# Optimization experiments

Measured on AMD Instinct MI355X. Metric: run time of the kernel, lower is better.

## Reference

```python
import jax, jax.numpy as jnp
import numpy as np

N_NODES = 100000


def gcn_conv(x, W, b, src, dst, n_nodes):
    # PyG GCNConv: h = x @ W; add self-loops; sym-normalized scatter-add; + bias
    loop = jnp.arange(n_nodes, dtype=src.dtype)
    src2 = jnp.concatenate([src, loop])
    dst2 = jnp.concatenate([dst, loop])
    deg = jax.ops.segment_sum(jnp.ones(src2.shape, x.dtype), dst2, num_segments=n_nodes)
    dinv = jax.lax.rsqrt(deg)  # deg >= 1 thanks to self-loops
    norm = dinv[src2] * dinv[dst2]                 # [E+N]
    h = x @ W                                      # [N, out]
    msg = h[src2] * norm[:, None]                  # gather + scale, [E+N, out]
    out = jax.ops.segment_sum(msg, dst2, num_segments=n_nodes)  # scatter-add
    return out + b


def setup_inputs() -> dict:
    key = jax.random.key(0)
    k1, k2, k3, k4, k5 = jax.random.split(key, 5)
    nfeat, nhid = 128, 64
    n_edges = 1600000
    x = jax.random.normal(k1, (N_NODES, nfeat), dtype=jnp.float32)
    edge_index = jax.random.randint(k2, (2, n_edges), 0, N_NODES, dtype=jnp.int64)
    W1 = jax.random.normal(k3, (nfeat, nhid), dtype=jnp.float32) / np.sqrt(nfeat)
    b1 = jnp.zeros((nhid,), jnp.float32)
    W2 = jax.random.normal(k4, (nhid, nhid), dtype=jnp.float32) / np.sqrt(nhid)
    b2 = jnp.zeros((nhid,), jnp.float32)
    return {"x": x, "edge_index": edge_index, "W1": W1, "b1": b1, "W2": W2, "b2": b2}


def reference(x, edge_index, W1, b1, W2, b2):
    # eval mode: dropout is identity
    src, dst = edge_index[0], edge_index[1]
    h = jax.nn.relu(gcn_conv(x, W1, b1, src, dst, N_NODES))
    residual = h
    out = jax.nn.relu(gcn_conv(h, W2, b2, src, dst, N_NODES))
    return out + residual
```

## Files before the change

kernel.cpp:

```cpp
#include <hip/hip_runtime.h>

#define N_NODES 100000
#define NDUMMY 100000
#define NH 64
#define NB 512
#define NPB 196
#define BCAP 4096
#define PBCAP 5760
#define EPB 8192


__device__ __forceinline__ unsigned short f2bf(float f) {
    union { float f; unsigned int i; } c;
    c.f = f;
    unsigned int b = c.i;
    b += 0x7FFFu + ((b >> 16) & 1u);
    return (unsigned short)(b >> 16);
}

__device__ __forceinline__ unsigned pack2bf(float lo, float hi) {
    return (unsigned)f2bf(lo) | ((unsigned)f2bf(hi) << 16);
}

__device__ __forceinline__ float bfLO(unsigned u) {
    union { unsigned i; float f; } c; c.i = u << 16; return c.f;
}
__device__ __forceinline__ float bfHI(unsigned u) {
    union { unsigned i; float f; } c; c.i = u & 0xFFFF0000u; return c.f;
}


__global__ __launch_bounds__(512) void k_init(int* __restrict__ bcur, unsigned* __restrict__ dummy_row) {
    int t = threadIdx.x;
    if (t < NB) bcur[t] = 0;
    if (t < 32) dummy_row[t] = 0;
}


__global__ __launch_bounds__(1024) void k_sort(const int* __restrict__ src, const int* __restrict__ dst,
                                               int* __restrict__ bcur, unsigned* __restrict__ ebuf, int e) {
    __shared__ unsigned sorted[EPB];
    __shared__ unsigned short cellof[EPB];
    __shared__ int lh[NB];
    __shared__ int lbase[NB];
    __shared__ int lcur[NB];
    __shared__ int gpos[NB];
    __shared__ int wsum[8];
    const int t = threadIdx.x;
    const int e0 = blockIdx.x * EPB;
    int cnt = e - e0; if (cnt > EPB) cnt = EPB;

    if (t < NB) lh[t] = 0;
    __syncthreads();

    for (int i = t * 4; i < cnt; i += 4096) {
        int4 d4 = *(const int4*)&dst[e0 + i];
        atomicAdd(&lh[d4.x / NPB], 1);
        atomicAdd(&lh[d4.y / NPB], 1);
        atomicAdd(&lh[d4.z / NPB], 1);
        atomicAdd(&lh[d4.w / NPB], 1);
    }
    __syncthreads();

    const int lane = t & 63, wave = t >> 6;
    int v = 0, inc = 0;
    if (t < NB) {
        v = lh[t];
        inc = v;
#pragma unroll
        for (int d = 1; d < 64; d <<= 1) {
            int u = __shfl_up(inc, d, 64);
            if (lane >= d) inc += u;
        }
        if (lane == 63) wsum[wave] = inc;
    }
    __syncthreads();
    if (t < NB) {
        int woff = 0;
#pragma unroll
        for (int w = 0; w < 8; ++w)
            if (w < wave) woff += wsum[w];
        const int excl = woff + inc - v;
        lbase[t] = excl;
        lcur[t] = excl;
        gpos[t] = atomicAdd(&bcur[t], v);
    }
    __syncthreads();

    for (int i = t * 4; i < cnt; i += 4096) {
        int4 d4 = *(const int4*)&dst[e0 + i];
        int4 s4 = *(const int4*)&src[e0 + i];
        int b0 = d4.x / NPB, b1 = d4.y / NPB, b2 = d4.z / NPB, b3 = d4.w / NPB;
        int p0 = atomicAdd(&lcur[b0], 1);
        int p1 = atomicAdd(&lcur[b1], 1);
        int p2 = atomicAdd(&lcur[b2], 1);
        int p3 = atomicAdd(&lcur[b3], 1);
        sorted[p0] = ((unsigned)(d4.x - b0 * NPB) << 17) | (unsigned)s4.x; cellof[p0] = (unsigned short)b0;
        sorted[p1] = ((unsigned)(d4.y - b1 * NPB) << 17) | (unsigned)s4.y; cellof[p1] = (unsigned short)b1;
        sorted[p2] = ((unsigned)(d4.z - b2 * NPB) << 17) | (unsigned)s4.z; cellof[p2] = (unsigned short)b2;
        sorted[p3] = ((unsigned)(d4.w - b3 * NPB) << 17) | (unsigned)s4.w; cellof[p3] = (unsigned short)b3;
    }
    __syncthreads();

    for (int i = t * 4; i < cnt; i += 4096) {
        uint4 sv = *(const uint4*)&sorted[i];
        ushort4 cv = *(const ushort4*)&cellof[i];
        int c0 = cv.x, c1 = cv.y, c2 = cv.z, c3 = cv.w;
        int g0 = gpos[c0] + (i + 0 - lbase[c0]);
        int g1 = gpos[c1] + (i + 1 - lbase[c1]);
        int g2 = gpos[c2] + (i + 2 - lbase[c2]);
        int g3 = gpos[c3] + (i + 3 - lbase[c3]);
        if (g0 < BCAP) ebuf[(long long)c0 * BCAP + g0] = sv.x;
        if (g1 < BCAP) ebuf[(long long)c1 * BCAP + g1] = sv.y;
        if (g2 < BCAP) ebuf[(long long)c2 * BCAP + g2] = sv.z;
        if (g3 < BCAP) ebuf[(long long)c3 * BCAP + g3] = sv.w;
    }
}

__global__ __launch_bounds__(256) void k_build(const unsigned* __restrict__ ebuf, const int* __restrict__ bcur,
                                               int* __restrict__ rowptr, int* __restrict__ degp,
                                               float* __restrict__ dinv, int* __restrict__ csrc, int n) {
    __shared__ unsigned ls[BCAP];
    __shared__ int lh[256];
    __shared__ int lpv[256];
    __shared__ int lstart[256];
    __shared__ int lc[256];
    __shared__ int wsum[4];
    const int b = blockIdx.x;
    const int t = threadIdx.x;
    const int node0 = b * NPB;
    int count = bcur[b];
    if (count > BCAP) count = BCAP;
    const int rbase = b * PBCAP;

    lh[t] = 0;
    for (int i = t; i < count; i += 256) ls[i] = ebuf[(long long)b * BCAP + i];
    __syncthreads();
    for (int i = t; i < count; i += 256) atomicAdd(&lh[ls[i] >> 17], 1);
    __syncthreads();

    const int v = lh[t];
    lpv[t] = (v + 7) & ~7;
    __syncthreads();
    const int g = t & ~3;
    const int pvg = max(max(lpv[g], lpv[g + 1]), max(lpv[g + 2], lpv[g + 3]));

    const int lane = t & 63, wave = t >> 6;
    int inc = pvg;
#pragma unroll
    for (int d = 1; d < 64; d <<= 1) {
        int u = __shfl_up(inc, d, 64);
        if (lane >= d) inc += u;
    }
    if (lane == 63) wsum[wave] = inc;
    __syncthreads();
    int woff = 0;
#pragma unroll
    for (int w = 0; w < 4; ++w)
        if (w < wave) woff += wsum[w];
    const int start = rbase + woff + inc - pvg;

    lstart[t] = start;
    lc[t] = start;
    const int node = node0 + t;
    if (t < NPB && node < n) {
        rowptr[node] = start;
        degp[node] = pvg;
        dinv[node] = rsqrtf((float)(v + 1));
    }
    __syncthreads();

    for (int i = t; i < count; i += 256) {
        unsigned u = ls[i];
        int pos = atomicAdd(&lc[u >> 17], 1);
        csrc[pos] = (int)(u & 0x1FFFFu);
    }
    __syncthreads();

    const int pend = lstart[t] + pvg;
    for (int p = lc[t]; p < pend; ++p) csrc[p] = NDUMMY;
}


template <int K>
__global__ __launch_bounds__(256) void k_gemm_scale(const float* __restrict__ X, const float* __restrict__ W,
                                                    const float* __restrict__ dinv,
                                                    unsigned short* __restrict__ out, int n) {
    __shared__ float xsT[64][68];
    __shared__ float ws[64][64];
    const int tid = threadIdx.x;
    const int n0 = blockIdx.x * 64;
    const int tc = tid & 15;
    const int tn = tid >> 4;

    float acc[4][4];
#pragma unroll
    for (int r = 0; r < 4; ++r)
#pragma unroll
        for (int c = 0; c < 4; ++c) acc[r][c] = 0.f;

    for (int kb = 0; kb < K; kb += 64) {
        for (int idx = tid * 4; idx < 4096; idx += 1024) {
            int r = idx >> 6, c = idx & 63;
            *(float4*)&ws[r][c] = *(const float4*)&W[(kb + r) * NH + c];
        }
        for (int idx = tid * 4; idx < 4096; idx += 1024) {
            int row = idx >> 6, c = idx & 63;
            float4 v = make_float4(0.f, 0.f, 0.f, 0.f);
            if (n0 + row < n) v = *(const float4*)&X[(long long)(n0 + row) * K + kb + c];
            xsT[c + 0][row] = v.x;
            xsT[c + 1][row] = v.y;
            xsT[c + 2][row] = v.z;
            xsT[c + 3][row] = v.w;
        }
        __syncthreads();

#pragma unroll 8
        for (int k = 0; k < 64; ++k) {
            float4 xa = *(const float4*)&xsT[k][tn * 4];
            float4 wa = *(const float4*)&ws[k][tc * 4];
            float xr[4] = {xa.x, xa.y, xa.z, xa.w};
            float wc[4] = {wa.x, wa.y, wa.z, wa.w};
#pragma unroll
            for (int r = 0; r < 4; ++r)
#pragma unroll
                for (int c = 0; c < 4; ++c) acc[r][c] += xr[r] * wc[c];
        }
        __syncthreads();
    }

#pragma unroll
    for (int r = 0; r < 4; ++r) {
        int node = n0 + 4 * tn + r;
        if (node < n) {
            float dv = dinv[node];
            ushort4 o;
            o.x = f2bf(acc[r][0] * dv);
            o.y = f2bf(acc[r][1] * dv);
            o.z = f2bf(acc[r][2] * dv);
            o.w = f2bf(acc[r][3] * dv);
            *(ushort4*)&out[(long long)node * NH + tc * 4] = o;
        }
    }
}


__global__ __launch_bounds__(256) void k_agg(const unsigned* __restrict__ hs32, const float* __restrict__ dinv,
                                             const int* __restrict__ rowptr, const int* __restrict__ degp,
                                             const int* __restrict__ csrc,
                                             const float* __restrict__ bias, const float* __restrict__ resid,
                                             float* __restrict__ out, int n) {
    const int gt = blockIdx.x * 256 + threadIdx.x;
    const int wave = gt >> 6;
    const int lane = threadIdx.x & 63;
    const int sub = lane >> 4;
    const int li = lane & 15;
    const int node = wave * 4 + sub;
    if (node >= n) return;

    const uint2* hsv = (const uint2*)hs32;
    uint2 su = hsv[node * 16 + li];
    float aLx = bfLO(su.x), aHx = bfHI(su.x), aLy = bfLO(su.y), aHy = bfHI(su.y);
    float bLx = 0.f, bHx = 0.f, bLy = 0.f, bHy = 0.f;

    const int rp = rowptr[node];
    const int dg = degp[node];
    for (int e = 0; e < dg; e += 8) {
        int4 c0 = *(const int4*)&csrc[rp + e];
        int4 c1 = *(const int4*)&csrc[rp + e + 4];
        uint2 u0 = hsv[c0.x * 16 + li];
        uint2 u1 = hsv[c0.y * 16 + li];
        uint2 u2 = hsv[c0.z * 16 + li];
        uint2 u3 = hsv[c0.w * 16 + li];
        uint2 u4 = hsv[c1.x * 16 + li];
        uint2 u5 = hsv[c1.y * 16 + li];
        uint2 u6 = hsv[c1.z * 16 + li];
        uint2 u7 = hsv[c1.w * 16 + li];
        aLx += bfLO(u0.x); aHx += bfHI(u0.x); aLy += bfLO(u0.y); aHy += bfHI(u0.y);
        bLx += bfLO(u1.x); bHx += bfHI(u1.x); bLy += bfLO(u1.y); bHy += bfHI(u1.y);
        aLx += bfLO(u2.x); aHx += bfHI(u2.x); aLy += bfLO(u2.y); aHy += bfHI(u2.y);
        bLx += bfLO(u3.x); bHx += bfHI(u3.x); bLy += bfLO(u3.y); bHy += bfHI(u3.y);
        aLx += bfLO(u4.x); aHx += bfHI(u4.x); aLy += bfLO(u4.y); aHy += bfHI(u4.y);
        bLx += bfLO(u5.x); bHx += bfHI(u5.x); bLy += bfLO(u5.y); bHy += bfHI(u5.y);
        aLx += bfLO(u6.x); aHx += bfHI(u6.x); aLy += bfLO(u6.y); aHy += bfHI(u6.y);
        bLx += bfLO(u7.x); bHx += bfHI(u7.x); bLy += bfLO(u7.y); bHy += bfHI(u7.y);
    }
    const float dv = dinv[node];
    const float4 bb = *(const float4*)&bias[4 * li];
    float v0 = fmaxf(dv * (aLx + bLx) + bb.x, 0.f);
    float v1 = fmaxf(dv * (aHx + bHx) + bb.y, 0.f);
    float v2 = fmaxf(dv * (aLy + bLy) + bb.z, 0.f);
    float v3 = fmaxf(dv * (aHy + bHy) + bb.w, 0.f);
    const long long ob = (long long)node * NH + 4 * li;
    if (resid) {
        float4 rr = *(const float4*)&resid[ob];
        v0 += rr.x; v1 += rr.y; v2 += rr.z; v3 += rr.w;
    }
    *(float4*)&out[ob] = make_float4(v0, v1, v2, v3);
}


extern "C" void kernel_launch(void* const* d_in, const int* in_sizes, int n_in,
                              void* d_out, int out_size, void* d_ws, size_t ws_size,
                              hipStream_t stream) {
    const float* x  = (const float*)d_in[0];
    const int*   ei = (const int*)d_in[1];
    const float* W1 = (const float*)d_in[2];
    const float* b1 = (const float*)d_in[3];
    const float* W2 = (const float*)d_in[4];
    const float* b2 = (const float*)d_in[5];
    float* out = (float*)d_out;

    const int N = N_NODES;
    const int E = in_sizes[1] / 2;
    const int* src = ei;
    const int* dst = ei + E;

    const int NP = 100352;
    int*   bcur   = (int*)d_ws;
    int*   rowptr = bcur + NB;
    int*   degp   = rowptr + NP;
    float* dinv   = (float*)(degp + NP);
    int*   csrc   = (int*)(dinv + NP);
    unsigned* ebuf = (unsigned*)(csrc + NB * PBCAP);
    unsigned* hs32 = ebuf;
    unsigned short* hsb = (unsigned short*)hs32;
    float* h1     = (float*)(hs32 + (long long)(NDUMMY + 1) * 32);

    const int nb_sort = (E + EPB - 1) / EPB;

    k_init<<<1, 512, 0, stream>>>(bcur, hs32 + (long long)NDUMMY * 32);
    k_sort<<<nb_sort, 1024, 0, stream>>>(src, dst, bcur, ebuf, E);
    k_build<<<NB, 256, 0, stream>>>(ebuf, bcur, rowptr, degp, dinv, csrc, N);

    k_gemm_scale<128><<<(N + 63) / 64, 256, 0, stream>>>(x, W1, dinv, hsb, N);
    k_agg<<<(N + 15) / 16, 256, 0, stream>>>(hs32, dinv, rowptr, degp, csrc, b1, nullptr, h1, N);

    k_gemm_scale<64><<<(N + 63) / 64, 256, 0, stream>>>(h1, W2, dinv, hsb, N);
    k_agg<<<(N + 15) / 16, 256, 0, stream>>>(hs32, dinv, rowptr, degp, csrc, b2, h1, out, N);
}
```

Measured before the change: 153.6 us.

## Replace FP32 SIMT GEMM with bf16 MFMA matrix-core GEMM

```diff
diff --git a/kernel.cpp b/kernel.cpp
--- a/kernel.cpp
+++ b/kernel.cpp
@@ -182,64 +182,80 @@
 }
 
 
+typedef __attribute__((ext_vector_type(8))) short bf16x8;
+typedef __attribute__((ext_vector_type(4))) float f32x4;
+
 template <int K>
-__global__ __launch_bounds__(256) void k_gemm_scale(const float* __restrict__ X, const float* __restrict__ W,
-                                                    const float* __restrict__ dinv,
-                                                    unsigned short* __restrict__ out, int n) {
-    __shared__ float xsT[64][68];
-    __shared__ float ws[64][64];
+__global__ __launch_bounds__(256, 3) void k_gemm_mfma(const float* __restrict__ X, const float* __restrict__ W,
+                                                      const float* __restrict__ dinv,
+                                                      unsigned short* __restrict__ out, int n) {
+    constexpr int KP = K + 8;
+    constexpr int NKS = K / 32;
+    __shared__ unsigned short xs[128][KP];
     const int tid = threadIdx.x;
-    const int n0 = blockIdx.x * 64;
-    const int tc = tid & 15;
-    const int tn = tid >> 4;
-
-    float acc[4][4];
-#pragma unroll
-    for (int r = 0; r < 4; ++r)
-#pragma unroll
-        for (int c = 0; c < 4; ++c) acc[r][c] = 0.f;
-
-    for (int kb = 0; kb < K; kb += 64) {
-        for (int idx = tid * 4; idx < 4096; idx += 1024) {
-            int r = idx >> 6, c = idx & 63;
-            *(float4*)&ws[r][c] = *(const float4*)&W[(kb + r) * NH + c];
+    const int lane = tid & 63;
+    const int wv = tid >> 6;
+    const int n0 = blockIdx.x * 128;
+    const int col = lane & 15;
+    const int krow = (lane >> 4) * 8;
+
+    for (int idx = tid * 4; idx < 128 * K; idx += 1024) {
+        int row = idx / K, c = idx % K;
+        float4 v = make_float4(0.f, 0.f, 0.f, 0.f);
+        if (n0 + row < n) v = *(const float4*)&X[(long long)(n0 + row) * K + c];
+        ushort4 o;
+        o.x = f2bf(v.x); o.y = f2bf(v.y); o.z = f2bf(v.z); o.w = f2bf(v.w);
+        *(ushort4*)&xs[row][c] = o;
+    }
+
+    union FragU { bf16x8 v; unsigned u[4]; };
+    bf16x8 wb[4][NKS];
+#pragma unroll
+    for (int nt = 0; nt < 4; ++nt) {
+#pragma unroll
+        for (int ks = 0; ks < NKS; ++ks) {
+            FragU f;
+#pragma unroll
+            for (int m = 0; m < 4; ++m) {
+                int k = ks * 32 + krow + 2 * m;
+                int c = nt * 16 + col;
+                f.u[m] = pack2bf(W[k * NH + c], W[(k + 1) * NH + c]);
+            }
+            wb[nt][ks] = f.v;
         }
-        for (int idx = tid * 4; idx < 4096; idx += 1024) {
-            int row = idx >> 6, c = idx & 63;
-            float4 v = make_float4(0.f, 0.f, 0.f, 0.f);
-            if (n0 + row < n) v = *(const float4*)&X[(long long)(n0 + row) * K + kb + c];
-            xsT[c + 0][row] = v.x;
-            xsT[c + 1][row] = v.y;
-            xsT[c + 2][row] = v.z;
-            xsT[c + 3][row] = v.w;
+    }
+    __syncthreads();
+
+    f32x4 zero = {0.f, 0.f, 0.f, 0.f};
+    f32x4 acc[2][4];
+#pragma unroll
+    for (int mt = 0; mt < 2; ++mt)
+#pragma unroll
+        for (int nt = 0; nt < 4; ++nt) acc[mt][nt] = zero;
+
+#pragma unroll
+    for (int ks = 0; ks < NKS; ++ks) {
+#pragma unroll
+        for (int mt = 0; mt < 2; ++mt) {
+            const int r = wv * 32 + mt * 16 + col;
+            bf16x8 a = *(const bf16x8*)&xs[r][ks * 32 + krow];
+#pragma unroll
+            for (int nt = 0; nt < 4; ++nt)
+                acc[mt][nt] = __builtin_amdgcn_mfma_f32_16x16x32_bf16(a, wb[nt][ks], acc[mt][nt], 0, 0, 0);
         }
-        __syncthreads();
-
-#pragma unroll 8
-        for (int k = 0; k < 64; ++k) {
-            float4 xa = *(const float4*)&xsT[k][tn * 4];
-            float4 wa = *(const float4*)&ws[k][tc * 4];
-            float xr[4] = {xa.x, xa.y, xa.z, xa.w};
-            float wc[4] = {wa.x, wa.y, wa.z, wa.w};
-#pragma unroll
-            for (int r = 0; r < 4; ++r)
-#pragma unroll
-                for (int c = 0; c < 4; ++c) acc[r][c] += xr[r] * wc[c];
-        }
-        __syncthreads();
-    }
-
-#pragma unroll
-    for (int r = 0; r < 4; ++r) {
-        int node = n0 + 4 * tn + r;
-        if (node < n) {
-            float dv = dinv[node];
-            ushort4 o;
-            o.x = f2bf(acc[r][0] * dv);
-            o.y = f2bf(acc[r][1] * dv);
-            o.z = f2bf(acc[r][2] * dv);
-            o.w = f2bf(acc[r][3] * dv);
-            *(ushort4*)&out[(long long)node * NH + tc * 4] = o;
+    }
+
+#pragma unroll
+    for (int mt = 0; mt < 2; ++mt) {
+#pragma unroll
+        for (int r = 0; r < 4; ++r) {
+            int node = n0 + wv * 32 + mt * 16 + (lane >> 4) * 4 + r;
+            if (node < n) {
+                float dv = dinv[node];
+#pragma unroll
+                for (int nt = 0; nt < 4; ++nt)
+                    out[(long long)node * NH + nt * 16 + col] = f2bf(acc[mt][nt][r] * dv);
+            }
         }
     }
 }
@@ -333,9 +349,9 @@
     k_sort<<<nb_sort, 1024, 0, stream>>>(src, dst, bcur, ebuf, E);
     k_build<<<NB, 256, 0, stream>>>(ebuf, bcur, rowptr, degp, dinv, csrc, N);
 
-    k_gemm_scale<128><<<(N + 63) / 64, 256, 0, stream>>>(x, W1, dinv, hsb, N);
+    k_gemm_mfma<128><<<(N + 127) / 128, 256, 0, stream>>>(x, W1, dinv, hsb, N);
     k_agg<<<(N + 15) / 16, 256, 0, stream>>>(hs32, dinv, rowptr, degp, csrc, b1, nullptr, h1, N);
 
-    k_gemm_scale<64><<<(N + 63) / 64, 256, 0, stream>>>(h1, W2, dinv, hsb, N);
+    k_gemm_mfma<64><<<(N + 127) / 128, 256, 0, stream>>>(h1, W2, dinv, hsb, N);
     k_agg<<<(N + 15) / 16, 256, 0, stream>>>(hs32, dinv, rowptr, degp, csrc, b2, h1, out, N);
 }
```

Result: faster. 135.3 us (-11.9%).
